# Performance work log

Measured on AMD Instinct MI355X. Metric: run time of the kernel, lower is better.

The kernel has to match this reference:

```python
import jax, jax.numpy as jnp
import numpy as np

T = 5            # Newton-Schulz iterations
NORM_GROUPS = 16 # groups along out_channels
EPS = 1e-5


def setup_inputs() -> dict:
    key = jax.random.key(0)
    # conv weight: [out_ch, in_ch, kh, kw]
    weight = jax.random.normal(key, (2048, 1024, 3, 3), dtype=jnp.float32) * 0.05
    return {"weight": weight}


def reference(weight):
    g = NORM_GROUPS
    out_ch = weight.shape[0]
    Z = weight.reshape(g, out_ch // g, -1)                 # [g, n, d]
    Zc = Z - Z.mean(axis=-1, keepdims=True)                # center each row
    S = jnp.einsum('gnd,gmd->gnm', Zc, Zc)                 # [g, n, n] covariance
    n = S.shape[-1]
    eye = jnp.eye(n, dtype=S.dtype)
    S = S + EPS * eye
    norm_S = jnp.sqrt(jnp.sum(S * S, axis=(1, 2), keepdims=True))  # fro norm, [g,1,1]
    S = S / norm_S

    B0 = jnp.broadcast_to(eye, S.shape)                    # B[0] = I

    def body(B, _):
        B3 = B @ B @ B                                     # matrix_power3
        Bn = 1.5 * B - 0.5 * (B3 @ S)                      # baddbmm(1.5, B, -0.5, B^3, S)
        return Bn, None

    Bt, _ = jax.lax.scan(body, B0, None, length=T)
    W = (Bt @ Zc) / jnp.sqrt(norm_S)                       # [g, n, d]
    return W.reshape(weight.shape)
```

## Files before the change

### kernel.cpp

```cpp
#include <hip/hip_runtime.h>


#define G 16
#define NROW 128
#define D 9216
#define OC 2048
#define KSPLIT 16
#define KCHUNK 576
#define EPSV 1e-5f

typedef float f32x16 __attribute__((ext_vector_type(16)));
typedef __bf16 bf16x8 __attribute__((ext_vector_type(8)));

union Frag {
    uint4 q;
    unsigned short s[8];
    bf16x8 v;
};

static __device__ __forceinline__ unsigned short f2bf(float x) {
    union { float f; unsigned int u; } a; a.f = x;
    unsigned int u = a.u;
    unsigned int r = u + 0x7FFFu + ((u >> 16) & 1u);
    return (unsigned short)(r >> 16);
}

static __device__ __forceinline__ float bf2f(unsigned short s) {
    union { unsigned int u; float f; } a; a.u = ((unsigned int)s) << 16;
    return a.f;
}

static __device__ __forceinline__ int swz(int r, int c) {
    return (r << 7) + ((((c >> 3) ^ (r & 15)) << 3) | (c & 7));
}

__global__ __launch_bounds__(256) void k_sgemm(const float* __restrict__ W,
                                               unsigned short* __restrict__ Zraw,
                                               float* __restrict__ Spart,
                                               float* __restrict__ rowsumPart) {
    __shared__ unsigned short tile[NROW * 128];
    __shared__ float rsum[NROW];
    int bid = blockIdx.x;
    int g = bid >> 4, ks = bid & 15;
    int t = threadIdx.x, lane = t & 63, wave = t >> 6;
    int mq = (wave & 1) * 64, nq = (wave >> 1) * 64;
    int m = lane & 31, h = lane >> 5;

    if (t < 128) rsum[t] = 0.f;

    f32x16 acc[2][2];
#pragma unroll
    for (int i = 0; i < 2; i++)
#pragma unroll
        for (int j = 0; j < 2; j++)
#pragma unroll
            for (int z = 0; z < 16; z++) acc[i][j][z] = 0.f;

    float rs[16], rsh[8];
#pragma unroll
    for (int i = 0; i < 16; i++) rs[i] = 0.f;
#pragma unroll
    for (int i = 0; i < 8; i++) rsh[i] = 0.f;

    const float* wg = W + (size_t)g * NROW * D + ks * KCHUNK;
    unsigned short* zo = Zraw + (size_t)g * NROW * D + ks * KCHUNK;

    float4 pf[16];
#pragma unroll
    for (int p = 0; p < 16; p++) {
        int fl = p * 256 + t, r = fl >> 5, cf = fl & 31;
        pf[p] = *(const float4*)(wg + (size_t)r * D + cf * 4);
    }

    for (int step = 0; step < 5; step++) {
        __syncthreads();
        if (step < 4) {
            int dbase = step * 128;
#pragma unroll
            for (int p = 0; p < 16; p++) {
                int fl = p * 256 + t, r = fl >> 5, cf = fl & 31;
                float4 x = pf[p];
                rs[p] += x.x + x.y + x.z + x.w;
                ushort4 pk;
                pk.x = f2bf(x.x); pk.y = f2bf(x.y);
                pk.z = f2bf(x.z); pk.w = f2bf(x.w);
                *(ushort4*)(zo + (size_t)r * D + dbase + cf * 4) = pk;
                union { ushort4 s4; uint2 u; } cv; cv.s4 = pk;
                *(uint2*)(tile + swz(r, cf * 4)) = cv.u;
            }
        } else {
#pragma unroll
            for (int p = 0; p < 8; p++) {
                int fl = p * 256 + t, r = fl >> 4, cf = fl & 15;
                float4 x = pf[p];
                rsh[p] += x.x + x.y + x.z + x.w;
                ushort4 pk;
                pk.x = f2bf(x.x); pk.y = f2bf(x.y);
                pk.z = f2bf(x.z); pk.w = f2bf(x.w);
                *(ushort4*)(zo + (size_t)r * D + 512 + cf * 4) = pk;
                union { ushort4 s4; uint2 u; } cv; cv.s4 = pk;
                *(uint2*)(tile + swz(r, cf * 4)) = cv.u;
            }
        }
        __syncthreads();
        if (step < 3) {
            int dbase = (step + 1) * 128;
#pragma unroll
            for (int p = 0; p < 16; p++) {
                int fl = p * 256 + t, r = fl >> 5, cf = fl & 31;
                pf[p] = *(const float4*)(wg + (size_t)r * D + dbase + cf * 4);
            }
        } else if (step == 3) {
#pragma unroll
            for (int p = 0; p < 8; p++) {
                int fl = p * 256 + t, r = fl >> 4, cf = fl & 15;
                pf[p] = *(const float4*)(wg + (size_t)r * D + 512 + cf * 4);
            }
        }
        int kmax = (step < 4) ? 8 : 4;
#pragma unroll
        for (int kk = 0; kk < 8; kk++) {
            if (kk >= kmax) break;
            int kb = kk * 16 + h * 8;
            Frag a0, a1, b0, b1;
            a0.q = *(const uint4*)(tile + swz(mq + m, kb));
            a1.q = *(const uint4*)(tile + swz(mq + 32 + m, kb));
            b0.q = *(const uint4*)(tile + swz(nq + m, kb));
            b1.q = *(const uint4*)(tile + swz(nq + 32 + m, kb));
            acc[0][0] = __builtin_amdgcn_mfma_f32_32x32x16_bf16(a0.v, b0.v, acc[0][0], 0, 0, 0);
            acc[0][1] = __builtin_amdgcn_mfma_f32_32x32x16_bf16(a0.v, b1.v, acc[0][1], 0, 0, 0);
            acc[1][0] = __builtin_amdgcn_mfma_f32_32x32x16_bf16(a1.v, b0.v, acc[1][0], 0, 0, 0);
            acc[1][1] = __builtin_amdgcn_mfma_f32_32x32x16_bf16(a1.v, b1.v, acc[1][1], 0, 0, 0);
        }
    }
    float* sp = Spart + (size_t)bid * 16384;
#pragma unroll
    for (int i = 0; i < 2; i++)
#pragma unroll
        for (int j = 0; j < 2; j++)
#pragma unroll
            for (int reg = 0; reg < 16; reg++) {
                int row = (reg & 3) + 8 * (reg >> 2) + 4 * h;
                sp[(mq + i * 32 + row) * 128 + nq + j * 32 + m] = acc[i][j][reg];
            }
#pragma unroll
    for (int p = 0; p < 16; p++) atomicAdd(&rsum[p * 8 + (t >> 5)], rs[p]);
#pragma unroll
    for (int p = 0; p < 8; p++) atomicAdd(&rsum[p * 16 + (t >> 4)], rsh[p]);
    __syncthreads();
    if (t < 128) rowsumPart[bid * 128 + t] = rsum[t];
}

__global__ __launch_bounds__(256) void k_reduce(const float* __restrict__ Spart,
                                                const float* __restrict__ rowsumPart,
                                                float* __restrict__ Sred,
                                                float* __restrict__ normPart) {
    __shared__ float muv[128];
    __shared__ float ls[4];
    int b = blockIdx.x;
    int g = b >> 4, part = b & 15;
    int t = threadIdx.x;
    if (t < 128) {
        float s = 0.f;
        for (int ks = 0; ks < KSPLIT; ks++) s += rowsumPart[(g * 16 + ks) * 128 + t];
        muv[t] = s * (1.0f / 9216.0f);
    }
    __syncthreads();
    int el = part * 1024 + t * 4;
    float4 s = {0.f, 0.f, 0.f, 0.f};
    for (int ks = 0; ks < KSPLIT; ks++) {
        float4 p = *(const float4*)(Spart + (size_t)(g * KSPLIT + ks) * 16384 + el);
        s.x += p.x; s.y += p.y; s.z += p.z; s.w += p.w;
    }
    int r = el >> 7, c = el & 127;
    float4 mc = *(float4*)&muv[c];
    float dm = 9216.0f * muv[r];
    s.x -= dm * mc.x; s.y -= dm * mc.y; s.z -= dm * mc.z; s.w -= dm * mc.w;
    if (r >= c && r <= c + 3) {
        if (r == c) s.x += EPSV;
        else if (r == c + 1) s.y += EPSV;
        else if (r == c + 2) s.z += EPSV;
        else s.w += EPSV;
    }
    *(float4*)(Sred + (size_t)g * 16384 + el) = s;
    float sq = s.x * s.x + s.y * s.y + s.z * s.z + s.w * s.w;
#pragma unroll
    for (int o = 32; o > 0; o >>= 1) sq += __shfl_down(sq, o, 64);
    if ((t & 63) == 0) ls[t >> 6] = sq;
    __syncthreads();
    if (t == 0) normPart[b] = ls[0] + ls[1] + ls[2] + ls[3];
}

__global__ __launch_bounds__(512) void k_ns(const float* __restrict__ Sred,
                                            const float* __restrict__ normPart,
                                            const float* __restrict__ rowsumPart,
                                            unsigned short* __restrict__ Bt,
                                            float* __restrict__ cvec) {
    extern __shared__ unsigned short sm[];
    unsigned short* Bb = sm;
    unsigned short* Sb = sm + 16384;
    unsigned short* Ub = sm + 32768;
    unsigned short* Vt = sm + 49152;
    int g = blockIdx.x;
    int t = threadIdx.x, lane = t & 63, wave = t >> 6;
    int m = lane & 31, h = lane >> 5;

    float ns = 0.f;
#pragma unroll
    for (int i = 0; i < 16; i++) ns += normPart[g * 16 + i];
    float rn = 1.0f / sqrtf(ns);

    {
        int r = t >> 2, c0 = (t & 3) * 32;
        const float* sp = Sred + (size_t)g * 16384 + r * 128 + c0;
#pragma unroll
        for (int q = 0; q < 4; q++) {
            int c = c0 + q * 8;
            float4 x0 = *(const float4*)(sp + q * 8);
            float4 x1 = *(const float4*)(sp + q * 8 + 4);
            float vv[8] = {x0.x, x0.y, x0.z, x0.w, x1.x, x1.y, x1.z, x1.w};
            Frag fs, fb;
#pragma unroll
            for (int i = 0; i < 8; i++) {
                float sv = vv[i] * rn;
                fs.s[i] = f2bf(sv);
                float bv = -0.5f * sv + ((r == c + i) ? 1.5f : 0.f);
                fb.s[i] = f2bf(bv);
            }
            *(uint4*)(Sb + swz(r, c)) = fs.q;
            *(uint4*)(Bb + swz(r, c)) = fb.q;
        }
    }
    Frag fI[2];
#pragma unroll
    for (int kk2 = 0; kk2 < 2; kk2++)
#pragma unroll
        for (int j = 0; j < 8; j++)
            fI[kk2].s[j] = (m == kk2 * 16 + h * 8 + j) ? (unsigned short)0x3FC0
                                                       : (unsigned short)0;
    __syncthreads();

    for (int iter = 0; iter < 4; iter++) {
#pragma unroll
        for (int i = 0; i < 4; i++) {
            int task = wave * 4 + i;
            int tmb = ((task >> 2) & 3) * 32, tnb = (task & 3) * 32;
            const unsigned short* Bsrc = (task < 16) ? Bb : Sb;
            unsigned short* dst = (task < 16) ? Ub : Vt;
            float sc = (task < 16) ? 1.0f : -0.5f;
            f32x16 acc;
#pragma unroll
            for (int z = 0; z < 16; z++) acc[z] = 0.f;
#pragma unroll
            for (int kk = 0; kk < 8; kk++) {
                Frag a, bfr;
                a.q = *(const uint4*)(Bb + swz(tmb + m, kk * 16 + h * 8));
                bfr.q = *(const uint4*)(Bsrc + swz(tnb + m, kk * 16 + h * 8));
                acc = __builtin_amdgcn_mfma_f32_32x32x16_bf16(a.v, bfr.v, acc, 0, 0, 0);
            }
#pragma unroll
            for (int q = 0; q < 4; q++) {
                union { unsigned short s[4]; uint2 u; } pk;
#pragma unroll
                for (int j = 0; j < 4; j++) pk.s[j] = f2bf(sc * acc[q * 4 + j]);
                *(uint2*)(dst + swz(tnb + m, tmb + q * 8 + h * 4)) = pk.u;
            }
        }
        __syncthreads();
        f32x16 acc2[2];
#pragma unroll
        for (int i = 0; i < 2; i++) {
            int task = wave * 2 + i;
            int tmb = (task >> 2) * 32, tnb = (task & 3) * 32;
#pragma unroll
            for (int z = 0; z < 16; z++) acc2[i][z] = 0.f;
#pragma unroll
            for (int kk = 0; kk < 8; kk++) {
                Frag a, bfr;
                a.q = *(const uint4*)(Ub + swz(tmb + m, kk * 16 + h * 8));
                bfr.q = *(const uint4*)(Vt + swz(tnb + m, kk * 16 + h * 8));
                acc2[i] = __builtin_amdgcn_mfma_f32_32x32x16_bf16(a.v, bfr.v, acc2[i], 0, 0, 0);
            }
#pragma unroll
            for (int kk2 = 0; kk2 < 2; kk2++) {
                Frag bfr;
                bfr.q = *(const uint4*)(Bb + swz(tnb + m, tmb + kk2 * 16 + h * 8));
                acc2[i] = __builtin_amdgcn_mfma_f32_32x32x16_bf16(fI[kk2].v, bfr.v, acc2[i], 0, 0, 0);
            }
        }
        __syncthreads();
#pragma unroll
        for (int i = 0; i < 2; i++) {
            int task = wave * 2 + i;
            int tmb = (task >> 2) * 32, tnb = (task & 3) * 32;
#pragma unroll
            for (int q = 0; q < 4; q++) {
                union { unsigned short s[4]; uint2 u; } pk;
#pragma unroll
                for (int j = 0; j < 4; j++) pk.s[j] = f2bf(acc2[i][q * 4 + j]);
                *(uint2*)(Bb + swz(tnb + m, tmb + q * 8 + h * 4)) = pk.u;
            }
        }
        __syncthreads();
    }
    {
        int r = t >> 2, c0 = (t & 3) * 32;
        unsigned short* bp = Bt + (size_t)g * 16384 + r * 128;
#pragma unroll
        for (int q = 0; q < 4; q++) {
            uint4 dd = *(const uint4*)(Bb + swz(r, c0 + q * 8));
            *(uint4*)(bp + c0 + q * 8) = dd;
        }
    }
    float* muv = (float*)(sm + 32768);
    if (t < 128) {
        float s = 0.f;
        for (int ks = 0; ks < KSPLIT; ks++) s += rowsumPart[(g * 16 + ks) * 128 + t];
        muv[t] = s * (1.0f / 9216.0f);
    }
    __syncthreads();
    if (t < 128) {
        float cacc = 0.f;
        for (int k = 0; k < 128; k++) cacc += bf2f(Bb[swz(t, k)]) * muv[k];
        cvec[g * 128 + t] = cacc;
    }
}

__global__ __launch_bounds__(256) void k_wgemm(const unsigned short* __restrict__ Zraw,
                                               const unsigned short* __restrict__ Bt,
                                               const float* __restrict__ normPart,
                                               const float* __restrict__ cvec,
                                               float* __restrict__ out) {
    __shared__ unsigned short Ab[16384];
    __shared__ unsigned short Zt[16384];
    __shared__ float cs[128];
    int nt = blockIdx.x, g = blockIdx.y;
    int t = threadIdx.x, lane = t & 63, wave = t >> 6;
    int m = lane & 31, h = lane >> 5;

    float nsum = 0.f;
#pragma unroll
    for (int i = 0; i < 16; i++) nsum += normPart[g * 16 + i];
    float ss = 1.0f / sqrtf(sqrtf(nsum));

    const unsigned short* bg = Bt + (size_t)g * 16384;
    const unsigned short* zg = Zraw + (size_t)g * NROW * D + nt * 128;
#pragma unroll
    for (int p = 0; p < 8; p++) {
        int flat = p * 256 + t;
        int r = flat >> 4, gc = flat & 15;
        uint4 da = *(const uint4*)(bg + r * 128 + gc * 8);
        uint4 dz = *(const uint4*)(zg + (size_t)r * D + gc * 8);
        *(uint4*)(Ab + swz(r, gc * 8)) = da;
        *(uint4*)(Zt + swz(r, gc * 8)) = dz;
    }
    if (t < 128) cs[t] = cvec[g * 128 + t] * ss;
    __syncthreads();

    int cw = wave * 32 + m;

    f32x16 acc[4];
#pragma unroll
    for (int i = 0; i < 4; i++)
#pragma unroll
        for (int z = 0; z < 16; z++) acc[i][z] = 0.f;

#pragma unroll
    for (int ks = 0; ks < 8; ks++) {
        int k0 = ks * 16 + h * 8;
        Frag b;
#pragma unroll
        for (int j = 0; j < 8; j++) b.s[j] = Zt[swz(k0 + j, cw)];
#pragma unroll
        for (int i = 0; i < 4; i++) {
            Frag a;
            a.q = *(const uint4*)(Ab + swz(i * 32 + m, k0));
            acc[i] = __builtin_amdgcn_mfma_f32_32x32x16_bf16(a.v, b.v, acc[i], 0, 0, 0);
        }
    }
    float* og = out + (size_t)(g * NROW) * D + nt * 128 + cw;
#pragma unroll
    for (int i = 0; i < 4; i++)
#pragma unroll
        for (int reg = 0; reg < 16; reg++) {
            int row = i * 32 + (reg & 3) + 8 * (reg >> 2) + 4 * h;
            og[(size_t)row * D] = acc[i][reg] * ss - cs[row];
        }
}

extern "C" void kernel_launch(void* const* d_in, const int* in_sizes, int n_in,
                              void* d_out, int out_size, void* d_ws, size_t ws_size,
                              hipStream_t stream) {
    const float* W = (const float*)d_in[0];
    float* out = (float*)d_out;
    char* ws = (char*)d_ws;

    unsigned short* Zraw = (unsigned short*)(ws);
    float* Spart = (float*)(ws + 37748736ULL);
    float* Sred = (float*)(ws + 54525952ULL);
    float* normPart = (float*)(ws + 55574528ULL);
    unsigned short* Bt = (unsigned short*)(ws + 55575552ULL);
    float* rowsumPart = (float*)(ws + 56099840ULL);
    float* cvec = (float*)(ws + 56230912ULL);

    k_sgemm<<<G * KSPLIT, 256, 0, stream>>>(W, Zraw, Spart, rowsumPart);
    k_reduce<<<256, 256, 0, stream>>>(Spart, rowsumPart, Sred, normPart);
    hipFuncSetAttribute((const void*)k_ns,
                        hipFuncAttributeMaxDynamicSharedMemorySize, 131072);
    k_ns<<<G, 512, 131072, stream>>>(Sred, normPart, rowsumPart, Bt, cvec);
    k_wgemm<<<dim3(72, G), 256, 0, stream>>>(Zraw, Bt, normPart, cvec, out);
}
```

Measured before the change: 187.7 us.

## Split S-gemm K-chunk across two wave sets per block with LDS reduction

The covariance kernel now runs 512 threads per block, split into two sets of four waves. Each set processes half of the 576-wide K chunk in its own LDS tile, and the two partial accumulators are summed through shared memory before a single write to Spart. The goal is more latency hiding per block and a shorter serial load/convert/MFMA loop on this 256-block grid. The cost is twice the LDS tile, higher per-block register pressure, and an extra LDS reduction step.

```diff
diff --git a/kernel.cpp b/kernel.cpp
--- a/kernel.cpp
+++ b/kernel.cpp
@@ -7,6 +7,7 @@
 #define OC 2048
 #define KSPLIT 16
 #define KCHUNK 576
+#define SETC 288
 #define EPSV 1e-5f
 
 typedef float f32x16 __attribute__((ext_vector_type(16)));
@@ -34,17 +35,21 @@
     return (r << 7) + ((((c >> 3) ^ (r & 15)) << 3) | (c & 7));
 }
 
-__global__ __launch_bounds__(256) void k_sgemm(const float* __restrict__ W,
+__global__ __launch_bounds__(512) void k_sgemm(const float* __restrict__ W,
                                                unsigned short* __restrict__ Zraw,
                                                float* __restrict__ Spart,
                                                float* __restrict__ rowsumPart) {
-    __shared__ unsigned short tile[NROW * 128];
+    __shared__ unsigned short tile[2][NROW * 128];
     __shared__ float rsum[NROW];
     int bid = blockIdx.x;
     int g = bid >> 4, ks = bid & 15;
     int t = threadIdx.x, lane = t & 63, wave = t >> 6;
-    int mq = (wave & 1) * 64, nq = (wave >> 1) * 64;
+    int set = wave >> 2;
+    int ts = t & 255;
+    int w4 = wave & 3;
+    int mq = (w4 & 1) * 64, nq = (w4 >> 1) * 64;
     int m = lane & 31, h = lane >> 5;
+    unsigned short* tl = tile[set];
 
     if (t < 128) rsum[t] = 0.f;
 
@@ -56,29 +61,29 @@
 #pragma unroll
             for (int z = 0; z < 16; z++) acc[i][j][z] = 0.f;
 
-    float rs[16], rsh[8];
+    float rs[16], rq[4];
 #pragma unroll
     for (int i = 0; i < 16; i++) rs[i] = 0.f;
 #pragma unroll
-    for (int i = 0; i < 8; i++) rsh[i] = 0.f;
-
-    const float* wg = W + (size_t)g * NROW * D + ks * KCHUNK;
-    unsigned short* zo = Zraw + (size_t)g * NROW * D + ks * KCHUNK;
+    for (int i = 0; i < 4; i++) rq[i] = 0.f;
+
+    const float* wg = W + (size_t)g * NROW * D + ks * KCHUNK + set * SETC;
+    unsigned short* zo = Zraw + (size_t)g * NROW * D + ks * KCHUNK + set * SETC;
 
     float4 pf[16];
 #pragma unroll
     for (int p = 0; p < 16; p++) {
-        int fl = p * 256 + t, r = fl >> 5, cf = fl & 31;
+        int fl = p * 256 + ts, r = fl >> 5, cf = fl & 31;
         pf[p] = *(const float4*)(wg + (size_t)r * D + cf * 4);
     }
 
-    for (int step = 0; step < 5; step++) {
+    for (int step = 0; step < 3; step++) {
         __syncthreads();
-        if (step < 4) {
+        if (step < 2) {
             int dbase = step * 128;
 #pragma unroll
             for (int p = 0; p < 16; p++) {
-                int fl = p * 256 + t, r = fl >> 5, cf = fl & 31;
+                int fl = p * 256 + ts, r = fl >> 5, cf = fl & 31;
                 float4 x = pf[p];
                 rs[p] += x.x + x.y + x.z + x.w;
                 ushort4 pk;
@@ -86,69 +91,85 @@
                 pk.z = f2bf(x.z); pk.w = f2bf(x.w);
                 *(ushort4*)(zo + (size_t)r * D + dbase + cf * 4) = pk;
                 union { ushort4 s4; uint2 u; } cv; cv.s4 = pk;
-                *(uint2*)(tile + swz(r, cf * 4)) = cv.u;
+                *(uint2*)(tl + swz(r, cf * 4)) = cv.u;
             }
         } else {
 #pragma unroll
-            for (int p = 0; p < 8; p++) {
-                int fl = p * 256 + t, r = fl >> 4, cf = fl & 15;
+            for (int p = 0; p < 4; p++) {
+                int fl = p * 256 + ts, r = fl >> 3, cf = fl & 7;
                 float4 x = pf[p];
-                rsh[p] += x.x + x.y + x.z + x.w;
+                rq[p] += x.x + x.y + x.z + x.w;
                 ushort4 pk;
                 pk.x = f2bf(x.x); pk.y = f2bf(x.y);
                 pk.z = f2bf(x.z); pk.w = f2bf(x.w);
-                *(ushort4*)(zo + (size_t)r * D + 512 + cf * 4) = pk;
+                *(ushort4*)(zo + (size_t)r * D + 256 + cf * 4) = pk;
                 union { ushort4 s4; uint2 u; } cv; cv.s4 = pk;
-                *(uint2*)(tile + swz(r, cf * 4)) = cv.u;
+                *(uint2*)(tl + swz(r, cf * 4)) = cv.u;
             }
         }
         __syncthreads();
-        if (step < 3) {
-            int dbase = (step + 1) * 128;
+        if (step == 0) {
 #pragma unroll
             for (int p = 0; p < 16; p++) {
-                int fl = p * 256 + t, r = fl >> 5, cf = fl & 31;
-                pf[p] = *(const float4*)(wg + (size_t)r * D + dbase + cf * 4);
-            }
-        } else if (step == 3) {
-#pragma unroll
-            for (int p = 0; p < 8; p++) {
-                int fl = p * 256 + t, r = fl >> 4, cf = fl & 15;
-                pf[p] = *(const float4*)(wg + (size_t)r * D + 512 + cf * 4);
-            }
-        }
-        int kmax = (step < 4) ? 8 : 4;
+                int fl = p * 256 + ts, r = fl >> 5, cf = fl & 31;
+                pf[p] = *(const float4*)(wg + (size_t)r * D + 128 + cf * 4);
+            }
+        } else if (step == 1) {
+#pragma unroll
+            for (int p = 0; p < 4; p++) {
+                int fl = p * 256 + ts, r = fl >> 3, cf = fl & 7;
+                pf[p] = *(const float4*)(wg + (size_t)r * D + 256 + cf * 4);
+            }
+        }
+        int kmax = (step < 2) ? 8 : 2;
 #pragma unroll
         for (int kk = 0; kk < 8; kk++) {
             if (kk >= kmax) break;
             int kb = kk * 16 + h * 8;
             Frag a0, a1, b0, b1;
-            a0.q = *(const uint4*)(tile + swz(mq + m, kb));
-            a1.q = *(const uint4*)(tile + swz(mq + 32 + m, kb));
-            b0.q = *(const uint4*)(tile + swz(nq + m, kb));
-            b1.q = *(const uint4*)(tile + swz(nq + 32 + m, kb));
+            a0.q = *(const uint4*)(tl + swz(mq + m, kb));
+            a1.q = *(const uint4*)(tl + swz(mq + 32 + m, kb));
+            b0.q = *(const uint4*)(tl + swz(nq + m, kb));
+            b1.q = *(const uint4*)(tl + swz(nq + 32 + m, kb));
             acc[0][0] = __builtin_amdgcn_mfma_f32_32x32x16_bf16(a0.v, b0.v, acc[0][0], 0, 0, 0);
             acc[0][1] = __builtin_amdgcn_mfma_f32_32x32x16_bf16(a0.v, b1.v, acc[0][1], 0, 0, 0);
             acc[1][0] = __builtin_amdgcn_mfma_f32_32x32x16_bf16(a1.v, b0.v, acc[1][0], 0, 0, 0);
             acc[1][1] = __builtin_amdgcn_mfma_f32_32x32x16_bf16(a1.v, b1.v, acc[1][1], 0, 0, 0);
         }
     }
-    float* sp = Spart + (size_t)bid * 16384;
-#pragma unroll
-    for (int i = 0; i < 2; i++)
-#pragma unroll
-        for (int j = 0; j < 2; j++)
-#pragma unroll
-            for (int reg = 0; reg < 16; reg++) {
-                int row = (reg & 3) + 8 * (reg >> 2) + 4 * h;
-                sp[(mq + i * 32 + row) * 128 + nq + j * 32 + m] = acc[i][j][reg];
-            }
-#pragma unroll
-    for (int p = 0; p < 16; p++) atomicAdd(&rsum[p * 8 + (t >> 5)], rs[p]);
-#pragma unroll
-    for (int p = 0; p < 8; p++) atomicAdd(&rsum[p * 16 + (t >> 4)], rsh[p]);
-    __syncthreads();
+#pragma unroll
+    for (int p = 0; p < 16; p++) atomicAdd(&rsum[p * 8 + (ts >> 5)], rs[p]);
+#pragma unroll
+    for (int p = 0; p < 4; p++) atomicAdd(&rsum[p * 32 + (ts >> 3)], rq[p]);
+
+    __syncthreads();
+    float* Sf = (float*)tile;
+    if (set == 0) {
+#pragma unroll
+        for (int i = 0; i < 2; i++)
+#pragma unroll
+            for (int j = 0; j < 2; j++)
+#pragma unroll
+                for (int reg = 0; reg < 16; reg++) {
+                    int row = mq + i * 32 + (reg & 3) + 8 * (reg >> 2) + 4 * h;
+                    Sf[row * 128 + nq + j * 32 + m] = acc[i][j][reg];
+                }
+    }
     if (t < 128) rowsumPart[bid * 128 + t] = rsum[t];
+    __syncthreads();
+    if (set == 1) {
+        float* sp = Spart + (size_t)bid * 16384;
+#pragma unroll
+        for (int i = 0; i < 2; i++)
+#pragma unroll
+            for (int j = 0; j < 2; j++)
+#pragma unroll
+                for (int reg = 0; reg < 16; reg++) {
+                    int row = mq + i * 32 + (reg & 3) + 8 * (reg >> 2) + 4 * h;
+                    int col = nq + j * 32 + m;
+                    sp[row * 128 + col] = acc[i][j][reg] + Sf[row * 128 + col];
+                }
+    }
 }
 
 __global__ __launch_bounds__(256) void k_reduce(const float* __restrict__ Spart,
@@ -403,7 +424,7 @@
     float* rowsumPart = (float*)(ws + 56099840ULL);
     float* cvec = (float*)(ws + 56230912ULL);
 
-    k_sgemm<<<G * KSPLIT, 256, 0, stream>>>(W, Zraw, Spart, rowsumPart);
+    k_sgemm<<<G * KSPLIT, 512, 0, stream>>>(W, Zraw, Spart, rowsumPart);
     k_reduce<<<256, 256, 0, stream>>>(Spart, rowsumPart, Sred, normPart);
     hipFuncSetAttribute((const void*)k_ns,
                         hipFuncAttributeMaxDynamicSharedMemorySize, 131072);
```

Result: slower. 208.6 us (+11.2%).

## Double-buffer sgemm LDS tile and fold split-K reduction into NS kernel

Applied to the files above, without the earlier changes.

The S-GEMM kernel now uses two LDS tiles, so the MFMA work on one chunk overlaps the conversion and store of the next, with one barrier per step instead of two. The separate k_reduce kernel is removed. Its split-K summation, mean correction, epsilon diagonal and Frobenius norm now run at the start of k_ns, which writes a per-group norm for k_wgemm. This saves a launch and the Sred round trip. The cost is that the reduction now runs on only 16 blocks instead of 256, which may serialize the 16 MB Spart read.

```diff
diff --git a/kernel.cpp b/kernel.cpp
--- a/kernel.cpp
+++ b/kernel.cpp
@@ -34,11 +34,11 @@
     return (r << 7) + ((((c >> 3) ^ (r & 15)) << 3) | (c & 7));
 }
 
-__global__ __launch_bounds__(256) void k_sgemm(const float* __restrict__ W,
-                                               unsigned short* __restrict__ Zraw,
-                                               float* __restrict__ Spart,
-                                               float* __restrict__ rowsumPart) {
-    __shared__ unsigned short tile[NROW * 128];
+__global__ __launch_bounds__(256, 1) void k_sgemm(const float* __restrict__ W,
+                                                  unsigned short* __restrict__ Zraw,
+                                                  float* __restrict__ Spart,
+                                                  float* __restrict__ rowsumPart) {
+    __shared__ unsigned short tile[2][NROW * 128];
     __shared__ float rsum[NROW];
     int bid = blockIdx.x;
     int g = bid >> 4, ks = bid & 15;
@@ -71,11 +71,57 @@
         int fl = p * 256 + t, r = fl >> 5, cf = fl & 31;
         pf[p] = *(const float4*)(wg + (size_t)r * D + cf * 4);
     }
-
-    for (int step = 0; step < 5; step++) {
-        __syncthreads();
-        if (step < 4) {
-            int dbase = step * 128;
+    {
+#pragma unroll
+        for (int p = 0; p < 16; p++) {
+            int fl = p * 256 + t, r = fl >> 5, cf = fl & 31;
+            float4 x = pf[p];
+            rs[p] += x.x + x.y + x.z + x.w;
+            ushort4 pk;
+            pk.x = f2bf(x.x); pk.y = f2bf(x.y);
+            pk.z = f2bf(x.z); pk.w = f2bf(x.w);
+            *(ushort4*)(zo + (size_t)r * D + cf * 4) = pk;
+            union { ushort4 s4; uint2 u; } cv; cv.s4 = pk;
+            *(uint2*)(tile[0] + swz(r, cf * 4)) = cv.u;
+        }
+    }
+    __syncthreads();
+
+#pragma unroll
+    for (int s = 0; s < 5; s++) {
+        if (s < 3) {
+            int dbase = (s + 1) * 128;
+#pragma unroll
+            for (int p = 0; p < 16; p++) {
+                int fl = p * 256 + t, r = fl >> 5, cf = fl & 31;
+                pf[p] = *(const float4*)(wg + (size_t)r * D + dbase + cf * 4);
+            }
+        } else if (s == 3) {
+#pragma unroll
+            for (int p = 0; p < 8; p++) {
+                int fl = p * 256 + t, r = fl >> 4, cf = fl & 15;
+                pf[p] = *(const float4*)(wg + (size_t)r * D + 512 + cf * 4);
+            }
+        }
+        const unsigned short* tl = tile[s & 1];
+        int kmax = (s < 4) ? 8 : 4;
+#pragma unroll
+        for (int kk = 0; kk < 8; kk++) {
+            if (kk >= kmax) break;
+            int kb = kk * 16 + h * 8;
+            Frag a0, a1, b0, b1;
+            a0.q = *(const uint4*)(tl + swz(mq + m, kb));
+            a1.q = *(const uint4*)(tl + swz(mq + 32 + m, kb));
+            b0.q = *(const uint4*)(tl + swz(nq + m, kb));
+            b1.q = *(const uint4*)(tl + swz(nq + 32 + m, kb));
+            acc[0][0] = __builtin_amdgcn_mfma_f32_32x32x16_bf16(a0.v, b0.v, acc[0][0], 0, 0, 0);
+            acc[0][1] = __builtin_amdgcn_mfma_f32_32x32x16_bf16(a0.v, b1.v, acc[0][1], 0, 0, 0);
+            acc[1][0] = __builtin_amdgcn_mfma_f32_32x32x16_bf16(a1.v, b0.v, acc[1][0], 0, 0, 0);
+            acc[1][1] = __builtin_amdgcn_mfma_f32_32x32x16_bf16(a1.v, b1.v, acc[1][1], 0, 0, 0);
+        }
+        if (s < 3) {
+            int dbase = (s + 1) * 128;
+            unsigned short* td = tile[(s + 1) & 1];
 #pragma unroll
             for (int p = 0; p < 16; p++) {
                 int fl = p * 256 + t, r = fl >> 5, cf = fl & 31;
@@ -86,9 +132,10 @@
                 pk.z = f2bf(x.z); pk.w = f2bf(x.w);
                 *(ushort4*)(zo + (size_t)r * D + dbase + cf * 4) = pk;
                 union { ushort4 s4; uint2 u; } cv; cv.s4 = pk;
-                *(uint2*)(tile + swz(r, cf * 4)) = cv.u;
-            }
-        } else {
+                *(uint2*)(td + swz(r, cf * 4)) = cv.u;
+            }
+        } else if (s == 3) {
+            unsigned short* td = tile[0];
 #pragma unroll
             for (int p = 0; p < 8; p++) {
                 int fl = p * 256 + t, r = fl >> 4, cf = fl & 15;
@@ -99,39 +146,10 @@
                 pk.z = f2bf(x.z); pk.w = f2bf(x.w);
                 *(ushort4*)(zo + (size_t)r * D + 512 + cf * 4) = pk;
                 union { ushort4 s4; uint2 u; } cv; cv.s4 = pk;
-                *(uint2*)(tile + swz(r, cf * 4)) = cv.u;
-            }
-        }
-        __syncthreads();
-        if (step < 3) {
-            int dbase = (step + 1) * 128;
-#pragma unroll
-            for (int p = 0; p < 16; p++) {
-                int fl = p * 256 + t, r = fl >> 5, cf = fl & 31;
-                pf[p] = *(const float4*)(wg + (size_t)r * D + dbase + cf * 4);
-            }
-        } else if (step == 3) {
-#pragma unroll
-            for (int p = 0; p < 8; p++) {
-                int fl = p * 256 + t, r = fl >> 4, cf = fl & 15;
-                pf[p] = *(const float4*)(wg + (size_t)r * D + 512 + cf * 4);
-            }
-        }
-        int kmax = (step < 4) ? 8 : 4;
-#pragma unroll
-        for (int kk = 0; kk < 8; kk++) {
-            if (kk >= kmax) break;
-            int kb = kk * 16 + h * 8;
-            Frag a0, a1, b0, b1;
-            a0.q = *(const uint4*)(tile + swz(mq + m, kb));
-            a1.q = *(const uint4*)(tile + swz(mq + 32 + m, kb));
-            b0.q = *(const uint4*)(tile + swz(nq + m, kb));
-            b1.q = *(const uint4*)(tile + swz(nq + 32 + m, kb));
-            acc[0][0] = __builtin_amdgcn_mfma_f32_32x32x16_bf16(a0.v, b0.v, acc[0][0], 0, 0, 0);
-            acc[0][1] = __builtin_amdgcn_mfma_f32_32x32x16_bf16(a0.v, b1.v, acc[0][1], 0, 0, 0);
-            acc[1][0] = __builtin_amdgcn_mfma_f32_32x32x16_bf16(a1.v, b0.v, acc[1][0], 0, 0, 0);
-            acc[1][1] = __builtin_amdgcn_mfma_f32_32x32x16_bf16(a1.v, b1.v, acc[1][1], 0, 0, 0);
-        }
+                *(uint2*)(td + swz(r, cf * 4)) = cv.u;
+            }
+        }
+        if (s < 4) __syncthreads();
     }
     float* sp = Spart + (size_t)bid * 16384;
 #pragma unroll
@@ -151,68 +169,65 @@
     if (t < 128) rowsumPart[bid * 128 + t] = rsum[t];
 }
 
-__global__ __launch_bounds__(256) void k_reduce(const float* __restrict__ Spart,
-                                                const float* __restrict__ rowsumPart,
-                                                float* __restrict__ Sred,
-                                                float* __restrict__ normPart) {
-    __shared__ float muv[128];
-    __shared__ float ls[4];
-    int b = blockIdx.x;
-    int g = b >> 4, part = b & 15;
-    int t = threadIdx.x;
-    if (t < 128) {
-        float s = 0.f;
-        for (int ks = 0; ks < KSPLIT; ks++) s += rowsumPart[(g * 16 + ks) * 128 + t];
-        muv[t] = s * (1.0f / 9216.0f);
-    }
-    __syncthreads();
-    int el = part * 1024 + t * 4;
-    float4 s = {0.f, 0.f, 0.f, 0.f};
-    for (int ks = 0; ks < KSPLIT; ks++) {
-        float4 p = *(const float4*)(Spart + (size_t)(g * KSPLIT + ks) * 16384 + el);
-        s.x += p.x; s.y += p.y; s.z += p.z; s.w += p.w;
-    }
-    int r = el >> 7, c = el & 127;
-    float4 mc = *(float4*)&muv[c];
-    float dm = 9216.0f * muv[r];
-    s.x -= dm * mc.x; s.y -= dm * mc.y; s.z -= dm * mc.z; s.w -= dm * mc.w;
-    if (r >= c && r <= c + 3) {
-        if (r == c) s.x += EPSV;
-        else if (r == c + 1) s.y += EPSV;
-        else if (r == c + 2) s.z += EPSV;
-        else s.w += EPSV;
-    }
-    *(float4*)(Sred + (size_t)g * 16384 + el) = s;
-    float sq = s.x * s.x + s.y * s.y + s.z * s.z + s.w * s.w;
-#pragma unroll
-    for (int o = 32; o > 0; o >>= 1) sq += __shfl_down(sq, o, 64);
-    if ((t & 63) == 0) ls[t >> 6] = sq;
-    __syncthreads();
-    if (t == 0) normPart[b] = ls[0] + ls[1] + ls[2] + ls[3];
-}
-
-__global__ __launch_bounds__(512) void k_ns(const float* __restrict__ Sred,
-                                            const float* __restrict__ normPart,
+__global__ __launch_bounds__(512) void k_ns(const float* __restrict__ Spart,
                                             const float* __restrict__ rowsumPart,
                                             unsigned short* __restrict__ Bt,
-                                            float* __restrict__ cvec) {
+                                            float* __restrict__ cvec,
+                                            float* __restrict__ gnorm) {
     extern __shared__ unsigned short sm[];
     unsigned short* Bb = sm;
     unsigned short* Sb = sm + 16384;
     unsigned short* Ub = sm + 32768;
     unsigned short* Vt = sm + 49152;
+    float* Sf = (float*)(sm + 32768);
+    float* muv0 = (float*)sm;
+    float* red = ((float*)sm) + 128;
     int g = blockIdx.x;
     int t = threadIdx.x, lane = t & 63, wave = t >> 6;
     int m = lane & 31, h = lane >> 5;
 
-    float ns = 0.f;
-#pragma unroll
-    for (int i = 0; i < 16; i++) ns += normPart[g * 16 + i];
+    if (t < 128) {
+        float s = 0.f;
+        for (int ks = 0; ks < KSPLIT; ks++) s += rowsumPart[(g * 16 + ks) * 128 + t];
+        muv0[t] = s * (1.0f / 9216.0f);
+    }
+    __syncthreads();
+
+    const float* sp0 = Spart + (size_t)g * KSPLIT * 16384;
+    float sq = 0.f;
+#pragma unroll
+    for (int q2 = 0; q2 < 8; q2++) {
+        int el = t * 32 + q2 * 4;
+        float4 s = {0.f, 0.f, 0.f, 0.f};
+        for (int ks = 0; ks < KSPLIT; ks++) {
+            float4 p = *(const float4*)(sp0 + (size_t)ks * 16384 + el);
+            s.x += p.x; s.y += p.y; s.z += p.z; s.w += p.w;
+        }
+        int r = el >> 7, c = el & 127;
+        float dm = 9216.0f * muv0[r];
+        s.x -= dm * muv0[c];     s.y -= dm * muv0[c + 1];
+        s.z -= dm * muv0[c + 2]; s.w -= dm * muv0[c + 3];
+        if (r >= c && r <= c + 3) {
+            if (r == c) s.x += EPSV;
+            else if (r == c + 1) s.y += EPSV;
+            else if (r == c + 2) s.z += EPSV;
+            else s.w += EPSV;
+        }
+        *(float4*)(Sf + el) = s;
+        sq += s.x * s.x + s.y * s.y + s.z * s.z + s.w * s.w;
+    }
+#pragma unroll
+    for (int o = 32; o > 0; o >>= 1) sq += __shfl_down(sq, o, 64);
+    if (lane == 0) red[wave] = sq;
+    __syncthreads();
+    float ns = red[0] + red[1] + red[2] + red[3] + red[4] + red[5] + red[6] + red[7];
+    if (t == 0) gnorm[g] = ns;
     float rn = 1.0f / sqrtf(ns);
+    __syncthreads();
 
     {
         int r = t >> 2, c0 = (t & 3) * 32;
-        const float* sp = Sred + (size_t)g * 16384 + r * 128 + c0;
+        const float* sp = Sf + r * 128 + c0;
 #pragma unroll
         for (int q = 0; q < 4; q++) {
             int c = c0 + q * 8;
@@ -328,7 +343,7 @@
 
 __global__ __launch_bounds__(256) void k_wgemm(const unsigned short* __restrict__ Zraw,
                                                const unsigned short* __restrict__ Bt,
-                                               const float* __restrict__ normPart,
+                                               const float* __restrict__ gnorm,
                                                const float* __restrict__ cvec,
                                                float* __restrict__ out) {
     __shared__ unsigned short Ab[16384];
@@ -338,10 +353,7 @@
     int t = threadIdx.x, lane = t & 63, wave = t >> 6;
     int m = lane & 31, h = lane >> 5;
 
-    float nsum = 0.f;
-#pragma unroll
-    for (int i = 0; i < 16; i++) nsum += normPart[g * 16 + i];
-    float ss = 1.0f / sqrtf(sqrtf(nsum));
+    float ss = 1.0f / sqrtf(sqrtf(gnorm[g]));
 
     const unsigned short* bg = Bt + (size_t)g * 16384;
     const unsigned short* zg = Zraw + (size_t)g * NROW * D + nt * 128;
@@ -397,16 +409,14 @@
 
     unsigned short* Zraw = (unsigned short*)(ws);
     float* Spart = (float*)(ws + 37748736ULL);
-    float* Sred = (float*)(ws + 54525952ULL);
-    float* normPart = (float*)(ws + 55574528ULL);
+    float* gnorm = (float*)(ws + 55574528ULL);
     unsigned short* Bt = (unsigned short*)(ws + 55575552ULL);
     float* rowsumPart = (float*)(ws + 56099840ULL);
     float* cvec = (float*)(ws + 56230912ULL);
 
     k_sgemm<<<G * KSPLIT, 256, 0, stream>>>(W, Zraw, Spart, rowsumPart);
-    k_reduce<<<256, 256, 0, stream>>>(Spart, rowsumPart, Sred, normPart);
     hipFuncSetAttribute((const void*)k_ns,
                         hipFuncAttributeMaxDynamicSharedMemorySize, 131072);
-    k_ns<<<G, 512, 131072, stream>>>(Sred, normPart, rowsumPart, Bt, cvec);
-    k_wgemm<<<dim3(72, G), 256, 0, stream>>>(Zraw, Bt, normPart, cvec, out);
-}
+    k_ns<<<G, 512, 131072, stream>>>(Spart, rowsumPart, Bt, cvec, gnorm);
+    k_wgemm<<<dim3(72, G), 256, 0, stream>>>(Zraw, Bt, gnorm, cvec, out);
+}
```

Result: slower. 244.2 us (+30.1%).
